# Kernel tuning notes

Hardware: AMD Instinct MI355X
Metric: run time of the kernel (lower is better)

The kernel has to match this reference:

```python
import jax, jax.numpy as jnp
import numpy as np

NEG_INF = jnp.float32(-1e9)  # finite large-negative avoids -inf*0 NaNs in grads


def setup_inputs() -> dict:
    key = jax.random.key(0)
    k1, k2, k3, k4, k5 = jax.random.split(key, 5)
    B, T, S, D = 16, 1024, 2048, 1024
    source = jax.random.normal(k1, (B, T, D), dtype=jnp.float32)
    memory_bank = jax.random.normal(k2, (B, S, D), dtype=jnp.float32)
    memory_lengths = jax.random.randint(k3, (B,), 1, S + 1, dtype=jnp.int32)
    # torch nn.Linear weights are [out_features, in_features]
    W_in = jax.random.normal(k4, (D, D), dtype=jnp.float32) / jnp.sqrt(jnp.float32(D))
    W_out = jax.random.normal(k5, (D, 2 * D), dtype=jnp.float32) / jnp.sqrt(jnp.float32(2 * D))
    return {"source": source, "memory_bank": memory_bank,
            "memory_lengths": memory_lengths, "W_in": W_in, "W_out": W_out}


def reference(source, memory_bank, memory_lengths, W_in, W_out):
    # GlobalAttention(attn_type='general', attn_func='softmax'), multi-step path
    B, T, D = source.shape
    S = memory_bank.shape[1]
    # score: general -> linear_in(h_t) @ h_s^T
    h_t = jnp.einsum('btd,ed->bte', source, W_in)            # [B,T,D]
    align = jnp.einsum('bte,bse->bts', h_t, memory_bank)      # [B,T,S]
    # sequence_mask on memory_lengths, broadcast over target dim
    mask = jnp.arange(S, dtype=jnp.int32)[None, None, :] < memory_lengths[:, None, None]
    align = jnp.where(mask, align, NEG_INF)
    align_vectors = jax.nn.softmax(align, axis=-1)            # [B,T,S]
    c = jnp.einsum('bts,bsd->btd', align_vectors, memory_bank)  # [B,T,D]
    concat_c = jnp.concatenate([c, source], axis=-1)          # [B,T,2D]
    attn_h = jnp.einsum('btf,of->bto', concat_c, W_out)       # linear_out, no bias for 'general'
    attn_h = jnp.tanh(attn_h)
    # not one_step -> transpose to [T,B,*]
    return attn_h.transpose(1, 0, 2), align_vectors.transpose(1, 0, 2)
```

## Files before the change

kernel.cpp:

```cpp
#include <hip/hip_runtime.h>

typedef __attribute__((ext_vector_type(8))) short s16x8;
typedef __attribute__((ext_vector_type(4))) float f32x4;
typedef __attribute__((ext_vector_type(4))) unsigned short u16x4;
typedef unsigned short u16;

__device__ __forceinline__ u16 f2bf(float x) {
  unsigned u = __builtin_bit_cast(unsigned, x);
  u = u + 0x7fffu + ((u >> 16) & 1u);
  return (u16)(u >> 16);
}
__device__ __forceinline__ float bf2f(u16 h) {
  return __builtin_bit_cast(float, (unsigned)h << 16);
}
__device__ __forceinline__ void split_bf(float x, u16 &h, u16 &l) {
  h = f2bf(x); l = f2bf(x - bf2f(h));
}

typedef __attribute__((address_space(1))) const unsigned int as1c_u32;
typedef __attribute__((address_space(3))) unsigned int as3_u32;
__device__ __forceinline__ void gload16(const void* g, void* l) {
  __builtin_amdgcn_global_load_lds((as1c_u32*)g, (as3_u32*)l, 16, 0, 0);
}

__global__ __launch_bounds__(256) void split_copy_k(
    const float* __restrict__ in, u16* __restrict__ oh, u16* __restrict__ ol, long n4) {
  const long i = (long)blockIdx.x * 256 + threadIdx.x;
  if (i >= n4) return;
  const f32x4 v = *(const f32x4*)(in + i * 4);
  u16x4 h, l;
#pragma unroll
  for (int e = 0; e < 4; ++e) { u16 hh, ll; split_bf(v[e], hh, ll); h[e] = hh; l[e] = ll; }
  *(u16x4*)(oh + i * 4) = h;
  *(u16x4*)(ol + i * 4) = l;
}

__global__ __launch_bounds__(256) void split_hi_k(
    const float* __restrict__ in, u16* __restrict__ oh, long n4) {
  const long i = (long)blockIdx.x * 256 + threadIdx.x;
  if (i >= n4) return;
  const f32x4 v = *(const f32x4*)(in + i * 4);
  u16x4 h;
#pragma unroll
  for (int e = 0; e < 4; ++e) h[e] = f2bf(v[e]);
  *(u16x4*)(oh + i * 4) = h;
}

__global__ __launch_bounds__(256) void transpose_bf_k(
    const u16* __restrict__ in, u16* __restrict__ outT) {
  __shared__ u16 tile[64][72];
  const int b = blockIdx.z;
  const int s0 = blockIdx.x * 64, d0 = blockIdx.y * 64;
  const u16* pin = in + (long)b * 2048 * 1024;
  u16* pout = outT + (long)b * 1024 * 2048;
  const int t = threadIdx.x;
#pragma unroll
  for (int i = 0; i < 4; ++i) {
    const int idx = i * 256 + t;
    const int r = idx >> 4;
    const int c4 = (idx & 15) * 4;
    *(u16x4*)&tile[r][c4] = *(const u16x4*)&pin[(long)(s0 + r) * 1024 + d0 + c4];
  }
  __syncthreads();
#pragma unroll
  for (int i = 0; i < 4; ++i) {
    const int idx = i * 256 + t;
    const int r = idx >> 4;
    const int c4 = (idx & 15) * 4;
    u16x4 v = { tile[c4][r], tile[c4 + 1][r], tile[c4 + 2][r], tile[c4 + 3][r] };
    *(u16x4*)&pout[(long)(d0 + r) * 2048 + s0 + c4] = v;
  }
}

__global__ __launch_bounds__(256) void softmax_k(
    float* __restrict__ alignBuf, const int* __restrict__ lens, float* __restrict__ outP) {
  const int row = blockIdx.x;
  const int b = row >> 10;
  const int tt = row & 1023;
  const int len = lens[b];
  float* arow = alignBuf + (long)row * 2048;
  const int t = threadIdx.x;
  const int lane = t & 63, wv = t >> 6;
  float v[8];
  float mx = -3.0e38f;
#pragma unroll
  for (int j = 0; j < 8; ++j) {
    const int s = j * 256 + t;
    float x = arow[s];
    x = (s < len) ? x : -1.0e9f;
    v[j] = x;
    mx = fmaxf(mx, x);
  }
#pragma unroll
  for (int off = 32; off; off >>= 1) mx = fmaxf(mx, __shfl_xor(mx, off));
  __shared__ float redm[4], reds[4];
  if (lane == 0) redm[wv] = mx;
  __syncthreads();
  mx = fmaxf(fmaxf(redm[0], redm[1]), fmaxf(redm[2], redm[3]));
  float e[8]; float sum = 0.f;
#pragma unroll
  for (int j = 0; j < 8; ++j) { e[j] = __expf(v[j] - mx); sum += e[j]; }
#pragma unroll
  for (int off = 32; off; off >>= 1) sum += __shfl_xor(sum, off);
  if (lane == 0) reds[wv] = sum;
  __syncthreads();
  sum = reds[0] + reds[1] + reds[2] + reds[3];
  const float inv = 1.0f / sum;
  u16* ph = (u16*)arow;
  u16* pl = ph + 2048;
  float* orow = outP + ((long)tt * 16 + b) * 2048;
#pragma unroll
  for (int j = 0; j < 8; ++j) {
    const int s = j * 256 + t;
    const float pv = e[j] * inv;
    orow[s] = pv;
    u16 h, l; split_bf(pv, h, l);
    ph[s] = h; pl[s] = l;
  }
}

template<int NPROD, int EP, int MASK>
__global__ __launch_bounds__(256) void gemm128(
    const u16* __restrict__ Ah, const u16* __restrict__ Al,
    const u16* __restrict__ Ah2, const u16* __restrict__ Al2,
    int kSplitA, int lda, long sA,
    const u16* __restrict__ Bh, const u16* __restrict__ Bl, int ldb, long sB,
    int K, const int* __restrict__ lens,
    float* __restrict__ Cf, u16* __restrict__ Ch, u16* __restrict__ Cl,
    int ldc, long sC, int lgx, int lgxy, int nwg) {
  constexpr int NT = (NPROD >= 3) ? 4 : (NPROD == 2 ? 3 : 2);
  __shared__ __align__(16) u16 lds[NT][4096];

  const int orig = blockIdx.x;
  const int wg = (orig & 7) * (nwg >> 3) + (orig >> 3);
  const int bx = wg & ((1 << lgx) - 1);
  const int by = (wg >> lgx) & ((1 << (lgxy - lgx)) - 1);
  const int bz = wg >> lgxy;

  const long m0 = (long)by * 128;
  const long n0 = (long)bx * 128;

  int Klim = K;
  if constexpr (MASK == 1) {
    if (n0 >= lens[bz]) return;
  }

  const u16* pAh  = Ah  + (long)bz * sA;
  const u16* pAl  = Al  + (long)bz * sA;
  const u16* pAh2 = Ah2 + (long)bz * sA;
  const u16* pAl2 = Al2 + (long)bz * sA;
  const u16* pBh  = Bh  + (long)bz * sB;
  const u16* pBl  = Bl  + (long)bz * sB;

  const int t = threadIdx.x;
  const int lane = t & 63;
  const int wv = t >> 6;
  const int wm = wv >> 1;
  const int wn = wv & 1;
  const int lk = lane >> 4;
  const int lr = lane & 15;

  f32x4 acc[4][4];
#pragma unroll
  for (int i = 0; i < 4; ++i)
#pragma unroll
    for (int j = 0; j < 4; ++j) acc[i][j] = 0.0f;

  for (int k0 = 0; k0 < Klim; k0 += 32) {
    __syncthreads();
#pragma unroll
    for (int j = 0; j < 2; ++j) {
      const int ci = (j * 4 + wv) * 64;
      const int c = ci + lane;
      const int kc = c >> 7;
      const int r = c & 127;
      const int k = k0 + kc * 8;
      const u16 *aH = pAh, *aL = pAl;
      long ka = k;
      if (k >= kSplitA) { aH = pAh2; aL = pAl2; ka = k - kSplitA; }
      const long aoff = (m0 + r) * (long)lda + ka;
      gload16(aH + aoff, &lds[0][ci * 8]);
      if constexpr (NPROD >= 2) gload16(aL + aoff, &lds[2][ci * 8]);
      const long boff = (n0 + r) * (long)ldb + k;
      gload16(pBh + boff, &lds[1][ci * 8]);
      if constexpr (NPROD >= 3) gload16(pBl + boff, &lds[3][ci * 8]);
    }
    __syncthreads();

    s16x8 ah[4], al[4], bh[4], bl[4];
#pragma unroll
    for (int f = 0; f < 4; ++f) {
      const int ra = wm * 64 + f * 16 + lr;
      const int rb = wn * 64 + f * 16 + lr;
      ah[f] = *(const s16x8*)&lds[0][lk * 1024 + ra * 8];
      bh[f] = *(const s16x8*)&lds[1][lk * 1024 + rb * 8];
      if constexpr (NPROD >= 2) al[f] = *(const s16x8*)&lds[2][lk * 1024 + ra * 8];
      if constexpr (NPROD >= 3) bl[f] = *(const s16x8*)&lds[3][lk * 1024 + rb * 8];
    }
#pragma unroll
    for (int i = 0; i < 4; ++i)
#pragma unroll
      for (int j = 0; j < 4; ++j) {
        acc[i][j] = __builtin_amdgcn_mfma_f32_16x16x32_bf16(ah[i], bh[j], acc[i][j], 0, 0, 0);
        if constexpr (NPROD >= 3)
          acc[i][j] = __builtin_amdgcn_mfma_f32_16x16x32_bf16(ah[i], bl[j], acc[i][j], 0, 0, 0);
        if constexpr (NPROD >= 2)
          acc[i][j] = __builtin_amdgcn_mfma_f32_16x16x32_bf16(al[i], bh[j], acc[i][j], 0, 0, 0);
      }
  }

#pragma unroll
  for (int fm = 0; fm < 4; ++fm)
#pragma unroll
    for (int fn = 0; fn < 4; ++fn)
#pragma unroll
      for (int r = 0; r < 4; ++r) {
        const long row = m0 + wm * 64 + fm * 16 + (lane >> 4) * 4 + r;
        const long col = n0 + wn * 64 + fn * 16 + lr;
        const float v = acc[fm][fn][r];
        if constexpr (EP == 0) {
          Cf[(long)bz * sC + row * ldc + col] = v;
        } else if constexpr (EP == 1) {
          u16 h, l; split_bf(v, h, l);
          const long o = (long)bz * sC + row * ldc + col;
          Ch[o] = h; Cl[o] = l;
        }
      }
}

template<int NPROD, int EP, int MASK>
__global__ __launch_bounds__(256) void gemm128w(
    const u16* __restrict__ Ah, const u16* __restrict__ Al,
    const u16* __restrict__ Ah2, const u16* __restrict__ Al2,
    int kSplitA, int lda, long sA,
    const u16* __restrict__ Bh, const u16* __restrict__ Bl, int ldb, long sB,
    int K, const int* __restrict__ lens,
    float* __restrict__ Cf, u16* __restrict__ Ch, u16* __restrict__ Cl,
    int ldc, long sC, int lgx, int lgxy, int nwg) {
  constexpr int NT = (NPROD >= 3) ? 4 : (NPROD == 2 ? 3 : 2);
  __shared__ __align__(16) u16 lds[NT][8192];

  const int orig = blockIdx.x;
  const int wg = (orig & 7) * (nwg >> 3) + (orig >> 3);
  const int bx = wg & ((1 << lgx) - 1);
  const int by = (wg >> lgx) & ((1 << (lgxy - lgx)) - 1);
  const int bz = wg >> lgxy;

  const long m0 = (long)by * 128;
  const long n0 = (long)bx * 128;

  int Klim = K;
  if constexpr (MASK == 2) {
    const int kl = (lens[bz] + 63) & ~63;
    Klim = kl < K ? kl : K;
  }

  const u16* pAh  = Ah  + (long)bz * sA;
  const u16* pAl  = Al  + (long)bz * sA;
  const u16* pAh2 = Ah2 + (long)bz * sA;
  const u16* pAl2 = Al2 + (long)bz * sA;
  const u16* pBh  = Bh  + (long)bz * sB;
  const u16* pBl  = Bl  + (long)bz * sB;

  const int t = threadIdx.x;
  const int lane = t & 63;
  const int wv = t >> 6;
  const int wm = wv >> 1;
  const int wn = wv & 1;
  const int lk = lane >> 4;
  const int lr = lane & 15;

  f32x4 acc[4][4];
#pragma unroll
  for (int i = 0; i < 4; ++i)
#pragma unroll
    for (int j = 0; j < 4; ++j) acc[i][j] = 0.0f;

  for (int k0 = 0; k0 < Klim; k0 += 64) {
    __syncthreads();
#pragma unroll
    for (int j = 0; j < 4; ++j) {
      const int ci = (j * 4 + wv) * 64;
      const int c = ci + lane;
      const int kc = c >> 7;
      const int r = c & 127;
      const int k = k0 + kc * 8;
      const u16 *aH = pAh, *aL = pAl;
      long ka = k;
      if (k >= kSplitA) { aH = pAh2; aL = pAl2; ka = k - kSplitA; }
      const long aoff = (m0 + r) * (long)lda + ka;
      gload16(aH + aoff, &lds[0][ci * 8]);
      if constexpr (NPROD >= 2) gload16(aL + aoff, &lds[2][ci * 8]);
      const long boff = (n0 + r) * (long)ldb + k;
      gload16(pBh + boff, &lds[1][ci * 8]);
      if constexpr (NPROD >= 3) gload16(pBl + boff, &lds[3][ci * 8]);
    }
    __syncthreads();

#pragma unroll
    for (int ks = 0; ks < 2; ++ks) {
      const int fb = (ks * 4 + lk) * 1024;
      s16x8 ah[4], al[4], bh[4], bl[4];
#pragma unroll
      for (int f = 0; f < 4; ++f) {
        const int ra = wm * 64 + f * 16 + lr;
        const int rb = wn * 64 + f * 16 + lr;
        ah[f] = *(const s16x8*)&lds[0][fb + ra * 8];
        bh[f] = *(const s16x8*)&lds[1][fb + rb * 8];
        if constexpr (NPROD >= 2) al[f] = *(const s16x8*)&lds[2][fb + ra * 8];
        if constexpr (NPROD >= 3) bl[f] = *(const s16x8*)&lds[3][fb + rb * 8];
      }
#pragma unroll
      for (int i = 0; i < 4; ++i)
#pragma unroll
        for (int j = 0; j < 4; ++j) {
          acc[i][j] = __builtin_amdgcn_mfma_f32_16x16x32_bf16(ah[i], bh[j], acc[i][j], 0, 0, 0);
          if constexpr (NPROD >= 3)
            acc[i][j] = __builtin_amdgcn_mfma_f32_16x16x32_bf16(ah[i], bl[j], acc[i][j], 0, 0, 0);
          if constexpr (NPROD >= 2)
            acc[i][j] = __builtin_amdgcn_mfma_f32_16x16x32_bf16(al[i], bh[j], acc[i][j], 0, 0, 0);
        }
    }
  }

#pragma unroll
  for (int fm = 0; fm < 4; ++fm)
#pragma unroll
    for (int fn = 0; fn < 4; ++fn)
#pragma unroll
      for (int r = 0; r < 4; ++r) {
        const long row = m0 + wm * 64 + fm * 16 + (lane >> 4) * 4 + r;
        const long col = n0 + wn * 64 + fn * 16 + lr;
        const float v = acc[fm][fn][r];
        if constexpr (EP == 2) {
          const long bb = row >> 10;
          const long tt = row & 1023;
          Cf[(tt * 16 + bb) * (long)ldc + col] = tanhf(v);
        } else {
          Ch[(long)bz * sC + row * ldc + col] = f2bf(v);
        }
      }
}

extern "C" void kernel_launch(void* const* d_in, const int* in_sizes, int n_in,
                              void* d_out, int out_size, void* d_ws, size_t ws_size,
                              hipStream_t stream) {
  (void)in_sizes; (void)n_in; (void)out_size; (void)ws_size;
  const float* src = (const float*)d_in[0];
  const float* mb  = (const float*)d_in[1];
  const int*   lens= (const int*)d_in[2];
  const float* Wi  = (const float*)d_in[3];
  const float* Wo  = (const float*)d_in[4];
  float* out = (float*)d_out;

  char* p = (char*)d_ws;
  u16* mbS_hi  = (u16*)p;
  u16* mbS_lo  = (u16*)(p + (64L << 20));
  u16* srcU_hi = (u16*)(p + (128L << 20));
  u16* srcU_lo = (u16*)(p + (160L << 20));
  u16* htc_hi  = (u16*)(p + (192L << 20));
  u16* htc_lo  = (u16*)(p + (224L << 20));
  float* alignBuf = (float*)(p + (256L << 20));
  u16* Wi_hi = (u16*)alignBuf;
  u16* Wi_lo = Wi_hi + 1048576;
  u16* mbT   = mbS_lo;
  u16* Wo_hi = mbS_hi;

  dim3 blk(256);
  split_copy_k<<<dim3(32768), blk, 0, stream>>>(mb,  mbS_hi, mbS_lo, 8388608L);
  split_copy_k<<<dim3(16384), blk, 0, stream>>>(src, srcU_hi, srcU_lo, 4194304L);
  split_copy_k<<<dim3(1024),  blk, 0, stream>>>(Wi,  Wi_hi,  Wi_lo,  262144L);

  gemm128<3, 1, 0><<<dim3(1024), blk, 0, stream>>>(
      srcU_hi, srcU_lo, srcU_hi, srcU_lo, 1 << 30, 1024, 0L,
      Wi_hi, Wi_lo, 1024, 0L,
      1024, lens,
      nullptr, htc_hi, htc_lo, 1024, 0L,
      3, 10, 1024);

  gemm128<3, 0, 1><<<dim3(2048), blk, 0, stream>>>(
      htc_hi, htc_lo, htc_hi, htc_lo, 1 << 30, 1024, 1048576L,
      mbS_hi, mbS_lo, 1024, 2097152L,
      1024, lens,
      alignBuf, nullptr, nullptr, 2048, 2097152L,
      4, 7, 2048);

  softmax_k<<<dim3(16384), blk, 0, stream>>>(alignBuf, lens, out + 16777216L);

  transpose_bf_k<<<dim3(32, 16, 16), blk, 0, stream>>>(mbS_hi, mbT);
  split_hi_k<<<dim3(2048), blk, 0, stream>>>(Wo, Wo_hi, 524288L);

  gemm128w<2, 3, 2><<<dim3(1024), blk, 0, stream>>>(
      (const u16*)alignBuf, (const u16*)alignBuf + 2048,
      (const u16*)alignBuf, (const u16*)alignBuf + 2048, 1 << 30, 4096, 4194304L,
      mbT, mbT, 2048, 2097152L,
      2048, lens,
      nullptr, htc_hi, htc_hi, 1024, 1048576L,
      3, 6, 1024);

  gemm128w<1, 2, 0><<<dim3(1024), blk, 0, stream>>>(
      htc_hi, htc_hi, srcU_hi, srcU_hi, 1024, 1024, 0L,
      Wo_hi, Wo_hi, 2048, 0L,
      2048, lens,
      out, nullptr, nullptr, 1024, 0L,
      3, 10, 1024);
}
```

Measured before the change: 883.6 us.

## Double-buffer LDS tiles in GEMM kernels with vmcnt-based prefetch

Both split-bf16 GEMM kernels now keep two LDS buffers and issue the global-to-LDS loads for the next K tile before computing the current one. Completion is tracked with explicit s_waitcnt vmcnt counts and raw s_barrier, replacing the per-iteration __syncthreads pair. The goal is to overlap global memory latency with MFMA work. The cost is twice the LDS footprint per block, which can lower occupancy. The wait helper only emits waits for counts 0, 8 and 12, so some template instantiations may get no wait at all and read incomplete tiles.

```diff
diff --git a/kernel.cpp b/kernel.cpp
--- a/kernel.cpp
+++ b/kernel.cpp
@@ -21,6 +21,13 @@
 typedef __attribute__((address_space(3))) unsigned int as3_u32;
 __device__ __forceinline__ void gload16(const void* g, void* l) {
   __builtin_amdgcn_global_load_lds((as1c_u32*)g, (as3_u32*)l, 16, 0, 0);
+}
+
+template<int N> __device__ __forceinline__ void wait_vmcnt() {
+  if constexpr (N == 0)       asm volatile("s_waitcnt vmcnt(0)" ::: "memory");
+  else if constexpr (N == 8)  asm volatile("s_waitcnt vmcnt(8)" ::: "memory");
+  else if constexpr (N == 12) asm volatile("s_waitcnt vmcnt(12)" ::: "memory");
+  __builtin_amdgcn_sched_barrier(0);
 }
 
 __global__ __launch_bounds__(256) void split_copy_k(
@@ -129,7 +136,8 @@
     float* __restrict__ Cf, u16* __restrict__ Ch, u16* __restrict__ Cl,
     int ldc, long sC, int lgx, int lgxy, int nwg) {
   constexpr int NT = (NPROD >= 3) ? 4 : (NPROD == 2 ? 3 : 2);
-  __shared__ __align__(16) u16 lds[NT][4096];
+  constexpr int W = 2 * NT;
+  __shared__ __align__(16) u16 lds[2][NT][4096];
 
   const int orig = blockIdx.x;
   const int wg = (orig & 7) * (nwg >> 3) + (orig >> 3);
@@ -140,7 +148,6 @@
   const long m0 = (long)by * 128;
   const long n0 = (long)bx * 128;
 
-  int Klim = K;
   if constexpr (MASK == 1) {
     if (n0 >= lens[bz]) return;
   }
@@ -166,8 +173,7 @@
 #pragma unroll
     for (int j = 0; j < 4; ++j) acc[i][j] = 0.0f;
 
-  for (int k0 = 0; k0 < Klim; k0 += 32) {
-    __syncthreads();
+  auto stage = [&](int buf, int k0) {
 #pragma unroll
     for (int j = 0; j < 2; ++j) {
       const int ci = (j * 4 + wv) * 64;
@@ -179,23 +185,24 @@
       long ka = k;
       if (k >= kSplitA) { aH = pAh2; aL = pAl2; ka = k - kSplitA; }
       const long aoff = (m0 + r) * (long)lda + ka;
-      gload16(aH + aoff, &lds[0][ci * 8]);
-      if constexpr (NPROD >= 2) gload16(aL + aoff, &lds[2][ci * 8]);
+      gload16(aH + aoff, &lds[buf][0][ci * 8]);
+      if constexpr (NPROD >= 2) gload16(aL + aoff, &lds[buf][2][ci * 8]);
       const long boff = (n0 + r) * (long)ldb + k;
-      gload16(pBh + boff, &lds[1][ci * 8]);
-      if constexpr (NPROD >= 3) gload16(pBl + boff, &lds[3][ci * 8]);
+      gload16(pBh + boff, &lds[buf][1][ci * 8]);
+      if constexpr (NPROD >= 3) gload16(pBl + boff, &lds[buf][3][ci * 8]);
     }
-    __syncthreads();
-
+  };
+
+  auto compute = [&](int buf) {
     s16x8 ah[4], al[4], bh[4], bl[4];
 #pragma unroll
     for (int f = 0; f < 4; ++f) {
       const int ra = wm * 64 + f * 16 + lr;
       const int rb = wn * 64 + f * 16 + lr;
-      ah[f] = *(const s16x8*)&lds[0][lk * 1024 + ra * 8];
-      bh[f] = *(const s16x8*)&lds[1][lk * 1024 + rb * 8];
-      if constexpr (NPROD >= 2) al[f] = *(const s16x8*)&lds[2][lk * 1024 + ra * 8];
-      if constexpr (NPROD >= 3) bl[f] = *(const s16x8*)&lds[3][lk * 1024 + rb * 8];
+      ah[f] = *(const s16x8*)&lds[buf][0][lk * 1024 + ra * 8];
+      bh[f] = *(const s16x8*)&lds[buf][1][lk * 1024 + rb * 8];
+      if constexpr (NPROD >= 2) al[f] = *(const s16x8*)&lds[buf][2][lk * 1024 + ra * 8];
+      if constexpr (NPROD >= 3) bl[f] = *(const s16x8*)&lds[buf][3][lk * 1024 + rb * 8];
     }
 #pragma unroll
     for (int i = 0; i < 4; ++i)
@@ -207,6 +214,18 @@
         if constexpr (NPROD >= 2)
           acc[i][j] = __builtin_amdgcn_mfma_f32_16x16x32_bf16(al[i], bh[j], acc[i][j], 0, 0, 0);
       }
+  };
+
+  const int KT = K >> 5;
+  stage(0, 0);
+  int cur = 0;
+  for (int kt = 0; kt < KT; ++kt) {
+    if (kt + 1 < KT) { stage(cur ^ 1, (kt + 1) << 5); wait_vmcnt<W>(); }
+    else             { wait_vmcnt<0>(); }
+    __builtin_amdgcn_s_barrier();
+    compute(cur);
+    __builtin_amdgcn_s_barrier();
+    cur ^= 1;
   }
 
 #pragma unroll
@@ -238,7 +257,8 @@
     float* __restrict__ Cf, u16* __restrict__ Ch, u16* __restrict__ Cl,
     int ldc, long sC, int lgx, int lgxy, int nwg) {
   constexpr int NT = (NPROD >= 3) ? 4 : (NPROD == 2 ? 3 : 2);
-  __shared__ __align__(16) u16 lds[NT][8192];
+  constexpr int W = 4 * NT;
+  __shared__ __align__(16) u16 lds[2][NT][8192];
 
   const int orig = blockIdx.x;
   const int wg = (orig & 7) * (nwg >> 3) + (orig >> 3);
@@ -276,8 +296,7 @@
 #pragma unroll
     for (int j = 0; j < 4; ++j) acc[i][j] = 0.0f;
 
-  for (int k0 = 0; k0 < Klim; k0 += 64) {
-    __syncthreads();
+  auto stage = [&](int buf, int k0) {
 #pragma unroll
     for (int j = 0; j < 4; ++j) {
       const int ci = (j * 4 + wv) * 64;
@@ -289,14 +308,15 @@
       long ka = k;
       if (k >= kSplitA) { aH = pAh2; aL = pAl2; ka = k - kSplitA; }
       const long aoff = (m0 + r) * (long)lda + ka;
-      gload16(aH + aoff, &lds[0][ci * 8]);
-      if constexpr (NPROD >= 2) gload16(aL + aoff, &lds[2][ci * 8]);
+      gload16(aH + aoff, &lds[buf][0][ci * 8]);
+      if constexpr (NPROD >= 2) gload16(aL + aoff, &lds[buf][2][ci * 8]);
       const long boff = (n0 + r) * (long)ldb + k;
-      gload16(pBh + boff, &lds[1][ci * 8]);
-      if constexpr (NPROD >= 3) gload16(pBl + boff, &lds[3][ci * 8]);
+      gload16(pBh + boff, &lds[buf][1][ci * 8]);
+      if constexpr (NPROD >= 3) gload16(pBl + boff, &lds[buf][3][ci * 8]);
     }
-    __syncthreads();
-
+  };
+
+  auto compute = [&](int buf) {
 #pragma unroll
     for (int ks = 0; ks < 2; ++ks) {
       const int fb = (ks * 4 + lk) * 1024;
@@ -305,10 +325,10 @@
       for (int f = 0; f < 4; ++f) {
         const int ra = wm * 64 + f * 16 + lr;
         const int rb = wn * 64 + f * 16 + lr;
-        ah[f] = *(const s16x8*)&lds[0][fb + ra * 8];
-        bh[f] = *(const s16x8*)&lds[1][fb + rb * 8];
-        if constexpr (NPROD >= 2) al[f] = *(const s16x8*)&lds[2][fb + ra * 8];
-        if constexpr (NPROD >= 3) bl[f] = *(const s16x8*)&lds[3][fb + rb * 8];
+        ah[f] = *(const s16x8*)&lds[buf][0][fb + ra * 8];
+        bh[f] = *(const s16x8*)&lds[buf][1][fb + rb * 8];
+        if constexpr (NPROD >= 2) al[f] = *(const s16x8*)&lds[buf][2][fb + ra * 8];
+        if constexpr (NPROD >= 3) bl[f] = *(const s16x8*)&lds[buf][3][fb + rb * 8];
       }
 #pragma unroll
       for (int i = 0; i < 4; ++i)
@@ -321,6 +341,18 @@
             acc[i][j] = __builtin_amdgcn_mfma_f32_16x16x32_bf16(al[i], bh[j], acc[i][j], 0, 0, 0);
         }
     }
+  };
+
+  const int KT = Klim >> 6;
+  stage(0, 0);
+  int cur = 0;
+  for (int kt = 0; kt < KT; ++kt) {
+    if (kt + 1 < KT) { stage(cur ^ 1, (kt + 1) << 6); wait_vmcnt<W>(); }
+    else             { wait_vmcnt<0>(); }
+    __builtin_amdgcn_s_barrier();
+    compute(cur);
+    __builtin_amdgcn_s_barrier();
+    cur ^= 1;
   }
 
 #pragma unroll
```

New measurement: 896.8 us. No clear change (+1.5%).

## Switch context and output GEMMs to single-pass fp16 with 256x128 tiles

Applied to the files above, without the earlier changes.

Replaces the split-bf16 multi-product MFMA path in the P·V and output-projection GEMMs with single fp16 MFMA products. The softmax now writes fp16 probabilities. The memory bank is transposed straight from fp32 into fp16, and the source and W_out are converted to fp16. The GEMM kernel moves to 512 threads with 256x128 tiles to raise data reuse. This cuts MFMA work and the bandwidth spent on the lo halves, at the cost of fp16 precision and range risk compared with the bf16x2/x3 emulation.

```diff
diff --git a/kernel.cpp b/kernel.cpp
--- a/kernel.cpp
+++ b/kernel.cpp
@@ -1,6 +1,7 @@
 #include <hip/hip_runtime.h>
 
 typedef __attribute__((ext_vector_type(8))) short s16x8;
+typedef __attribute__((ext_vector_type(8))) _Float16 f16x8;
 typedef __attribute__((ext_vector_type(4))) float f32x4;
 typedef __attribute__((ext_vector_type(4))) unsigned short u16x4;
 typedef unsigned short u16;
@@ -15,6 +16,9 @@
 }
 __device__ __forceinline__ void split_bf(float x, u16 &h, u16 &l) {
   h = f2bf(x); l = f2bf(x - bf2f(h));
+}
+__device__ __forceinline__ u16 f2h(float x) {
+  return __builtin_bit_cast(u16, (_Float16)x);
 }
 
 typedef __attribute__((address_space(1))) const unsigned int as1c_u32;
@@ -35,40 +39,37 @@
   *(u16x4*)(ol + i * 4) = l;
 }
 
-__global__ __launch_bounds__(256) void split_hi_k(
+__global__ __launch_bounds__(256) void copy_f16_k(
     const float* __restrict__ in, u16* __restrict__ oh, long n4) {
   const long i = (long)blockIdx.x * 256 + threadIdx.x;
   if (i >= n4) return;
   const f32x4 v = *(const f32x4*)(in + i * 4);
   u16x4 h;
 #pragma unroll
-  for (int e = 0; e < 4; ++e) h[e] = f2bf(v[e]);
+  for (int e = 0; e < 4; ++e) h[e] = f2h(v[e]);
   *(u16x4*)(oh + i * 4) = h;
 }
 
-__global__ __launch_bounds__(256) void transpose_bf_k(
-    const u16* __restrict__ in, u16* __restrict__ outT) {
-  __shared__ u16 tile[64][72];
+__global__ __launch_bounds__(256) void transpose_f16_k(
+    const float* __restrict__ in, u16* __restrict__ oh) {
+  __shared__ float tile[64][65];
   const int b = blockIdx.z;
   const int s0 = blockIdx.x * 64, d0 = blockIdx.y * 64;
-  const u16* pin = in + (long)b * 2048 * 1024;
-  u16* pout = outT + (long)b * 1024 * 2048;
+  const float* pin = in + (long)b * 2048 * 1024;
   const int t = threadIdx.x;
 #pragma unroll
-  for (int i = 0; i < 4; ++i) {
+  for (int i = 0; i < 16; ++i) {
     const int idx = i * 256 + t;
-    const int r = idx >> 4;
-    const int c4 = (idx & 15) * 4;
-    *(u16x4*)&tile[r][c4] = *(const u16x4*)&pin[(long)(s0 + r) * 1024 + d0 + c4];
+    const int r = idx >> 6, c = idx & 63;
+    tile[r][c] = pin[(long)(s0 + r) * 1024 + d0 + c];
   }
   __syncthreads();
-#pragma unroll
-  for (int i = 0; i < 4; ++i) {
+  u16* poh = oh + (long)b * 1024 * 2048;
+#pragma unroll
+  for (int i = 0; i < 16; ++i) {
     const int idx = i * 256 + t;
-    const int r = idx >> 4;
-    const int c4 = (idx & 15) * 4;
-    u16x4 v = { tile[c4][r], tile[c4 + 1][r], tile[c4 + 2][r], tile[c4 + 3][r] };
-    *(u16x4*)&pout[(long)(d0 + r) * 2048 + s0 + c4] = v;
+    const int r = idx >> 6, c = idx & 63;
+    poh[(long)(d0 + r) * 2048 + s0 + c] = f2h(tile[c][r]);
   }
 }
 
@@ -107,15 +108,13 @@
   sum = reds[0] + reds[1] + reds[2] + reds[3];
   const float inv = 1.0f / sum;
   u16* ph = (u16*)arow;
-  u16* pl = ph + 2048;
   float* orow = outP + ((long)tt * 16 + b) * 2048;
 #pragma unroll
   for (int j = 0; j < 8; ++j) {
     const int s = j * 256 + t;
     const float pv = e[j] * inv;
     orow[s] = pv;
-    u16 h, l; split_bf(pv, h, l);
-    ph[s] = h; pl[s] = l;
+    ph[s] = f2h(pv);
   }
 }
 
@@ -140,7 +139,6 @@
   const long m0 = (long)by * 128;
   const long n0 = (long)bx * 128;
 
-  int Klim = K;
   if constexpr (MASK == 1) {
     if (n0 >= lens[bz]) return;
   }
@@ -166,7 +164,7 @@
 #pragma unroll
     for (int j = 0; j < 4; ++j) acc[i][j] = 0.0f;
 
-  for (int k0 = 0; k0 < Klim; k0 += 32) {
+  for (int k0 = 0; k0 < K; k0 += 32) {
     __syncthreads();
 #pragma unroll
     for (int j = 0; j < 2; ++j) {
@@ -228,17 +226,15 @@
       }
 }
 
-template<int NPROD, int EP, int MASK>
-__global__ __launch_bounds__(256) void gemm128w(
-    const u16* __restrict__ Ah, const u16* __restrict__ Al,
-    const u16* __restrict__ Ah2, const u16* __restrict__ Al2,
-    int kSplitA, int lda, long sA,
-    const u16* __restrict__ Bh, const u16* __restrict__ Bl, int ldb, long sB,
+template<int EP, int MASK>
+__global__ __launch_bounds__(512) void gemmW(
+    const u16* __restrict__ A1, const u16* __restrict__ A2, int kSplitA, int lda, long sA,
+    const u16* __restrict__ B, int ldb, long sB,
     int K, const int* __restrict__ lens,
-    float* __restrict__ Cf, u16* __restrict__ Ch, u16* __restrict__ Cl,
+    float* __restrict__ Cf, u16* __restrict__ Ch,
     int ldc, long sC, int lgx, int lgxy, int nwg) {
-  constexpr int NT = (NPROD >= 3) ? 4 : (NPROD == 2 ? 3 : 2);
-  __shared__ __align__(16) u16 lds[NT][8192];
+  __shared__ __align__(16) u16 ldsA[16384];
+  __shared__ __align__(16) u16 ldsB[8192];
 
   const int orig = blockIdx.x;
   const int wg = (orig & 7) * (nwg >> 3) + (orig >> 3);
@@ -246,7 +242,7 @@
   const int by = (wg >> lgx) & ((1 << (lgxy - lgx)) - 1);
   const int bz = wg >> lgxy;
 
-  const long m0 = (long)by * 128;
+  const long m0 = (long)by * 256;
   const long n0 = (long)bx * 128;
 
   int Klim = K;
@@ -255,12 +251,9 @@
     Klim = kl < K ? kl : K;
   }
 
-  const u16* pAh  = Ah  + (long)bz * sA;
-  const u16* pAl  = Al  + (long)bz * sA;
-  const u16* pAh2 = Ah2 + (long)bz * sA;
-  const u16* pAl2 = Al2 + (long)bz * sA;
-  const u16* pBh  = Bh  + (long)bz * sB;
-  const u16* pBl  = Bl  + (long)bz * sB;
+  const u16* pA1 = A1 + (long)bz * sA;
+  const u16* pA2 = A2 + (long)bz * sA;
+  const u16* pB  = B  + (long)bz * sB;
 
   const int t = threadIdx.x;
   const int lane = t & 63;
@@ -280,46 +273,42 @@
     __syncthreads();
 #pragma unroll
     for (int j = 0; j < 4; ++j) {
-      const int ci = (j * 4 + wv) * 64;
+      const int ci = (j * 8 + wv) * 64;
+      const int c = ci + lane;
+      const int kc = c >> 8;
+      const int r = c & 255;
+      const int k = k0 + kc * 8;
+      const u16* a = pA1; long ka = k;
+      if (k >= kSplitA) { a = pA2; ka = k - kSplitA; }
+      gload16(a + (m0 + r) * (long)lda + ka, &ldsA[ci * 8]);
+    }
+#pragma unroll
+    for (int j = 0; j < 2; ++j) {
+      const int ci = (j * 8 + wv) * 64;
       const int c = ci + lane;
       const int kc = c >> 7;
       const int r = c & 127;
       const int k = k0 + kc * 8;
-      const u16 *aH = pAh, *aL = pAl;
-      long ka = k;
-      if (k >= kSplitA) { aH = pAh2; aL = pAl2; ka = k - kSplitA; }
-      const long aoff = (m0 + r) * (long)lda + ka;
-      gload16(aH + aoff, &lds[0][ci * 8]);
-      if constexpr (NPROD >= 2) gload16(aL + aoff, &lds[2][ci * 8]);
-      const long boff = (n0 + r) * (long)ldb + k;
-      gload16(pBh + boff, &lds[1][ci * 8]);
-      if constexpr (NPROD >= 3) gload16(pBl + boff, &lds[3][ci * 8]);
+      gload16(pB + (n0 + r) * (long)ldb + k, &ldsB[ci * 8]);
     }
     __syncthreads();
 
 #pragma unroll
     for (int ks = 0; ks < 2; ++ks) {
-      const int fb = (ks * 4 + lk) * 1024;
-      s16x8 ah[4], al[4], bh[4], bl[4];
+      const int kc = ks * 4 + lk;
+      f16x8 a[4], b[4];
 #pragma unroll
       for (int f = 0; f < 4; ++f) {
         const int ra = wm * 64 + f * 16 + lr;
         const int rb = wn * 64 + f * 16 + lr;
-        ah[f] = *(const s16x8*)&lds[0][fb + ra * 8];
-        bh[f] = *(const s16x8*)&lds[1][fb + rb * 8];
-        if constexpr (NPROD >= 2) al[f] = *(const s16x8*)&lds[2][fb + ra * 8];
-        if constexpr (NPROD >= 3) bl[f] = *(const s16x8*)&lds[3][fb + rb * 8];
+        a[f] = *(const f16x8*)&ldsA[(kc * 256 + ra) * 8];
+        b[f] = *(const f16x8*)&ldsB[(kc * 128 + rb) * 8];
       }
 #pragma unroll
       for (int i = 0; i < 4; ++i)
 #pragma unroll
-        for (int j = 0; j < 4; ++j) {
-          acc[i][j] = __builtin_amdgcn_mfma_f32_16x16x32_bf16(ah[i], bh[j], acc[i][j], 0, 0, 0);
-          if constexpr (NPROD >= 3)
-            acc[i][j] = __builtin_amdgcn_mfma_f32_16x16x32_bf16(ah[i], bl[j], acc[i][j], 0, 0, 0);
-          if constexpr (NPROD >= 2)
-            acc[i][j] = __builtin_amdgcn_mfma_f32_16x16x32_bf16(al[i], bh[j], acc[i][j], 0, 0, 0);
-        }
+        for (int j = 0; j < 4; ++j)
+          acc[i][j] = __builtin_amdgcn_mfma_f32_16x16x32_f16(a[i], b[j], acc[i][j], 0, 0, 0);
     }
   }
 
@@ -337,7 +326,7 @@
           const long tt = row & 1023;
           Cf[(tt * 16 + bb) * (long)ldc + col] = tanhf(v);
         } else {
-          Ch[(long)bz * sC + row * ldc + col] = f2bf(v);
+          Ch[(long)bz * sC + row * ldc + col] = f2h(v);
         }
       }
 }
@@ -363,8 +352,9 @@
   float* alignBuf = (float*)(p + (256L << 20));
   u16* Wi_hi = (u16*)alignBuf;
   u16* Wi_lo = Wi_hi + 1048576;
-  u16* mbT   = mbS_lo;
-  u16* Wo_hi = mbS_hi;
+  u16* mbT    = mbS_lo;
+  u16* Wo_f16 = mbS_hi;
+  u16* srcF16 = mbS_hi + 2097152;
 
   dim3 blk(256);
   split_copy_k<<<dim3(32768), blk, 0, stream>>>(mb,  mbS_hi, mbS_lo, 8388608L);
@@ -387,21 +377,21 @@
 
   softmax_k<<<dim3(16384), blk, 0, stream>>>(alignBuf, lens, out + 16777216L);
 
-  transpose_bf_k<<<dim3(32, 16, 16), blk, 0, stream>>>(mbS_hi, mbT);
-  split_hi_k<<<dim3(2048), blk, 0, stream>>>(Wo, Wo_hi, 524288L);
-
-  gemm128w<2, 3, 2><<<dim3(1024), blk, 0, stream>>>(
-      (const u16*)alignBuf, (const u16*)alignBuf + 2048,
-      (const u16*)alignBuf, (const u16*)alignBuf + 2048, 1 << 30, 4096, 4194304L,
-      mbT, mbT, 2048, 2097152L,
+  transpose_f16_k<<<dim3(32, 16, 16), blk, 0, stream>>>(mb, mbT);
+  copy_f16_k<<<dim3(2048),  blk, 0, stream>>>(Wo,  Wo_f16, 524288L);
+  copy_f16_k<<<dim3(16384), blk, 0, stream>>>(src, srcF16, 4194304L);
+
+  gemmW<3, 2><<<dim3(512), dim3(512), 0, stream>>>(
+      (const u16*)alignBuf, (const u16*)alignBuf, 1 << 30, 4096, 4194304L,
+      mbT, 2048, 2097152L,
       2048, lens,
-      nullptr, htc_hi, htc_hi, 1024, 1048576L,
-      3, 6, 1024);
-
-  gemm128w<1, 2, 0><<<dim3(1024), blk, 0, stream>>>(
-      htc_hi, htc_hi, srcU_hi, srcU_hi, 1024, 1024, 0L,
-      Wo_hi, Wo_hi, 2048, 0L,
+      nullptr, htc_hi, 1024, 1048576L,
+      3, 5, 512);
+
+  gemmW<2, 0><<<dim3(512), dim3(512), 0, stream>>>(
+      htc_hi, srcF16, 1024, 1024, 0L,
+      Wo_f16, 2048, 0L,
       2048, lens,
-      out, nullptr, nullptr, 1024, 0L,
-      3, 10, 1024);
-}
+      out, nullptr, 1024, 0L,
+      3, 9, 512);
+}
```

After: 817.2 us. -7.5%, faster.
